# Performance work log

Measured on AMD Instinct MI355X. Metric: run time of the kernel, lower is better.

## Reference

```python
import jax, jax.numpy as jnp
import numpy as np

L = 6       # n_layers
D = 1024    # d_model
H = 16      # n_heads
HD = D // H
DF = 4096   # d_ff
E = 8       # n_experts
K = 2       # top_k
V = 32000   # vocab
B = 2
S = 1024    # seq_len == max_seq_len


def setup_inputs() -> dict:
    key = jax.random.key(0)
    ks = iter(jax.random.split(key, 40))
    n = lambda shape: jax.random.normal(next(ks), shape, dtype=jnp.float32) * 0.02
    return {
        'input_ids': jax.random.randint(next(ks), (B, S), 0, V),
        'tok_emb': n((V, D)),
        'pos_emb': n((S, D)),
        'attn_in_w': n((L, 3 * D, D)),   # packed q,k,v in_proj (torch MultiheadAttention)
        'attn_in_b': jnp.zeros((L, 3 * D), jnp.float32),
        'attn_out_w': n((L, D, D)),
        'attn_out_b': jnp.zeros((L, D), jnp.float32),
        'ln1_w': jnp.ones((L, D), jnp.float32),
        'ln1_b': jnp.zeros((L, D), jnp.float32),
        'ln2_w': jnp.ones((L, D), jnp.float32),
        'ln2_b': jnp.zeros((L, D), jnp.float32),
        'ffn_w1': n((L, DF, D)),
        'ffn_b1': jnp.zeros((L, DF), jnp.float32),
        'ffn_w2': n((L, D, DF)),
        'ffn_b2': jnp.zeros((L, D), jnp.float32),
        'gate_w': n((L // 2, E, D)),     # router gate for the 3 MoE (odd) layers
        'lnf_w': jnp.ones((D,), jnp.float32),
        'lnf_b': jnp.zeros((D,), jnp.float32),
        'head_w': n((V, D)),
    }


def _ln(x, w, b):
    m = x.mean(-1, keepdims=True)
    v = x.var(-1, keepdims=True)
    return (x - m) / jnp.sqrt(v + 1e-5) * w + b


def _mha(x, in_w, in_b, out_w, out_b):
    b_, s_, _ = x.shape
    qkv = x @ in_w.T + in_b
    q, k, v = jnp.split(qkv, 3, axis=-1)
    rs = lambda t: t.reshape(b_, s_, H, HD)
    q, k, v = rs(q), rs(k), rs(v)
    scores = jnp.einsum('bqhd,bkhd->bhqk', q, k) / np.sqrt(HD).astype(np.float32)
    causal = jnp.tril(jnp.ones((s_, s_), bool))
    scores = jnp.where(causal[None, None], scores, -jnp.inf)
    a = jax.nn.softmax(scores, axis=-1)
    o = jnp.einsum('bhqk,bkhd->bqhd', a, v).reshape(b_, s_, D)
    return o @ out_w.T + out_b


def reference(input_ids, tok_emb, pos_emb, attn_in_w, attn_in_b, attn_out_w,
              attn_out_b, ln1_w, ln1_b, ln2_w, ln2_b, ffn_w1, ffn_b1, ffn_w2,
              ffn_b2, gate_w, lnf_w, lnf_b, head_w):
    s = input_ids.shape[1]
    x = tok_emb[input_ids] + pos_emb[jnp.arange(s)][None]  # [B,S,D]
    aux = jnp.float32(0.0)
    for i in range(L):
        h = _ln(x + _mha(x, attn_in_w[i], attn_in_b[i], attn_out_w[i], attn_out_b[i]),
                ln1_w[i], ln1_b[i])
        ffn = jax.nn.relu(h @ ffn_w1[i].T + ffn_b1[i]) @ ffn_w2[i].T + ffn_b2[i]
        if i % 2 == 1:  # MoE layer; source shares ONE expert module across all experts
            gi = i // 2
            probs = jax.nn.softmax(h @ gate_w[gi].T, axis=-1)     # [B,S,E]
            topv, topi = jax.lax.top_k(probs, K)
            ffn = ffn * topv.sum(-1, keepdims=True)               # combine top-k weights
            me = probs.mean((0, 1))                               # mean gate prob per expert
            ce = jax.nn.one_hot(topi[..., 0], E, dtype=probs.dtype).mean((0, 1))
            aux = aux + E * jnp.sum(me * ce)                      # load-balancing aux loss
        x = _ln(h + ffn, ln2_w[i], ln2_b[i])
    x = _ln(x, lnf_w, lnf_b)
    logits = x @ head_w.T  # [B,S,V]
    return (logits, aux)
```

## Files before the change

### kernel.cpp

```cpp
#include <hip/hip_runtime.h>
#include <hip/hip_bf16.h>

typedef __hip_bfloat16 bf16;
typedef __bf16 bf16x8 __attribute__((ext_vector_type(8)));
typedef float f32x4 __attribute__((ext_vector_type(4)));
typedef short s16x8 __attribute__((ext_vector_type(8)));
typedef unsigned short u16;

#define NL 6
#define DM 1024
#define NH 16
#define HD 64
#define DF 4096
#define NE 8
#define NV 32000
#define NB 2
#define NS 1024
#define NT (NB*NS)

__device__ __forceinline__ float ldin(const void* p, long i, int isf32) {
    return isf32 ? ((const float*)p)[i]
                 : __bfloat162float(((const bf16*)p)[i]);
}

__global__ __launch_bounds__(256)
void cvt_k(const void* __restrict__ src, bf16* __restrict__ dst, long n,
           const u16* __restrict__ probe)
{
    int isf32 = (probe[0] != (u16)0x3F80);
    long stride = (long)gridDim.x * 256 * 8;
    for (long i = ((long)blockIdx.x * 256 + threadIdx.x) * 8; i < n; i += stride) {
        if (isf32) {
            const float* s = (const float*)src + i;
            f32x4 f0 = *(const f32x4*)s;
            f32x4 f1 = *(const f32x4*)(s + 4);
            s16x8 o;
            #pragma unroll
            for (int jj = 0; jj < 4; ++jj) {
                bf16 v0 = __float2bfloat16(f0[jj]);
                bf16 v1 = __float2bfloat16(f1[jj]);
                o[jj]   = *(short*)&v0;
                o[4+jj] = *(short*)&v1;
            }
            *(s16x8*)&dst[i] = o;
        } else {
            *(s16x8*)&dst[i] = *(const s16x8*)((const u16*)src + i);
        }
    }
}

template<int TMI, int WF32, int WB16, int RELU>
__global__ __launch_bounds__(256)
void gemm128(const u16* __restrict__ A, const u16* __restrict__ B,
             const void* __restrict__ bias, long biasoff,
             const u16* __restrict__ probe,
             float* __restrict__ Cf, bf16* __restrict__ Cb,
             int M, int N, int K, int lda, int ldb, int ldc, float alpha)
{
    int isf32 = (probe[0] != (u16)0x3F80);
    int bm = blockIdx.x, bn = blockIdx.y;

    __shared__ __align__(16) u16 As[TMI*32*64];
    __shared__ __align__(16) u16 Bs[128*64];

    int t = threadIdx.x;
    int lane = t & 63, wv = t >> 6;
    int wr = wv >> 1, wc = wv & 1;
    int rsel = lane & 15, grp = lane >> 4;

    f32x4 acc[TMI][4] = {};

    const u16* Ag = A + (long)(bm * (TMI*32)) * lda;
    const u16* Bg = B + (long)(bn * 128) * ldb;
    int sub = lane >> 3;
    int csw = ((lane & 7) ^ sub) * 8;

    for (int kt = 0; kt < K; kt += 64) {
        __syncthreads();
        #pragma unroll
        for (int i = 0; i < TMI; ++i) {
            int row = wv*(TMI*8) + i*8;
            __builtin_amdgcn_global_load_lds(
                (const __attribute__((address_space(1))) void*)(Ag + (long)(row + sub)*lda + kt + csw),
                (__attribute__((address_space(3))) void*)(As + row*64),
                16, 0, 0);
        }
        #pragma unroll
        for (int i = 0; i < 4; ++i) {
            int row = wv*32 + i*8;
            __builtin_amdgcn_global_load_lds(
                (const __attribute__((address_space(1))) void*)(Bg + (long)(row + sub)*ldb + kt + csw),
                (__attribute__((address_space(3))) void*)(Bs + row*64),
                16, 0, 0);
        }
        __syncthreads();
        #pragma unroll
        for (int kk = 0; kk < 2; ++kk) {
            int js = ((kk*4 + grp) ^ (rsel & 7)) * 8;
            bf16x8 af[TMI], bf[4];
            #pragma unroll
            for (int mi = 0; mi < TMI; ++mi)
                af[mi] = *(const bf16x8*)&As[(wr*(TMI*16) + mi*16 + rsel)*64 + js];
            #pragma unroll
            for (int ni = 0; ni < 4; ++ni)
                bf[ni] = *(const bf16x8*)&Bs[(wc*64 + ni*16 + rsel)*64 + js];
            #pragma unroll
            for (int mi = 0; mi < TMI; ++mi)
                #pragma unroll
                for (int ni = 0; ni < 4; ++ni)
                    acc[mi][ni] = __builtin_amdgcn_mfma_f32_16x16x32_bf16(
                        af[mi], bf[ni], acc[mi][ni], 0, 0, 0);
        }
    }

    #pragma unroll
    for (int mi = 0; mi < TMI; ++mi)
    #pragma unroll
    for (int ni = 0; ni < 4; ++ni)
    #pragma unroll
    for (int j = 0; j < 4; ++j) {
        int row = bm*(TMI*32) + wr*(TMI*16) + mi*16 + grp*4 + j;
        int col = bn*128 + wc*64 + ni*16 + rsel;
        float v = acc[mi][ni][j] * alpha;
        if (bias) v += ldin(bias, biasoff + col, isf32);
        if (RELU) v = fmaxf(v, 0.f);
        long ci = (long)row * ldc + col;
        if (WF32) Cf[ci] = v;
        if (WB16) Cb[ci] = __float2bfloat16(v);
    }
}

__global__ __launch_bounds__(256)
void gemm64f(const u16* __restrict__ A, const void* __restrict__ B,
             const u16* __restrict__ probe, float* __restrict__ Cf,
             int M, int N, int K, int lda, int ldb, int ldc)
{
    int isf32 = (probe[0] != (u16)0x3F80);
    int bn = blockIdx.x, bm = blockIdx.y;
    __shared__ __align__(16) u16 As[64*72];
    __shared__ __align__(16) u16 Bs[64*72];
    int t = threadIdx.x;
    int lane = t & 63, wv = t >> 6;
    int wm = (wv >> 1) * 32, wn = (wv & 1) * 32;
    int rsel = lane & 15, grp = lane >> 4;
    f32x4 acc[2][2] = {};
    const u16* Ag = A + (long)(bm * 64) * lda;
    int r0 = t >> 3, c8 = (t & 7) * 8;
    for (int kt = 0; kt < K; kt += 64) {
        __syncthreads();
        #pragma unroll
        for (int p = 0; p < 2; ++p) {
            int r = r0 + 32 * p;
            *(s16x8*)&As[r*72 + c8] = *(const s16x8*)(Ag + (long)r * lda + kt + c8);
        }
        if (isf32) {
            const float* Bg = (const float*)B + (long)(bn * 64) * ldb;
            #pragma unroll
            for (int p = 0; p < 2; ++p) {
                int r = r0 + 32 * p;
                const float* src = Bg + (long)r * ldb + kt + c8;
                f32x4 f0 = *(const f32x4*)src;
                f32x4 f1 = *(const f32x4*)(src + 4);
                s16x8 o8;
                #pragma unroll
                for (int jj = 0; jj < 4; ++jj) {
                    bf16 v0 = __float2bfloat16(f0[jj]);
                    bf16 v1 = __float2bfloat16(f1[jj]);
                    o8[jj]   = *(short*)&v0;
                    o8[4+jj] = *(short*)&v1;
                }
                *(s16x8*)&Bs[r*72 + c8] = o8;
            }
        } else {
            const u16* Bg = (const u16*)B + (long)(bn * 64) * ldb;
            #pragma unroll
            for (int p = 0; p < 2; ++p) {
                int r = r0 + 32 * p;
                *(s16x8*)&Bs[r*72 + c8] = *(const s16x8*)(Bg + (long)r * ldb + kt + c8);
            }
        }
        __syncthreads();
        #pragma unroll
        for (int kk = 0; kk < 64; kk += 32) {
            bf16x8 a0 = *(const bf16x8*)&As[(wm +      rsel)*72 + kk + grp*8];
            bf16x8 a1 = *(const bf16x8*)&As[(wm + 16 + rsel)*72 + kk + grp*8];
            bf16x8 b0 = *(const bf16x8*)&Bs[(wn +      rsel)*72 + kk + grp*8];
            bf16x8 b1 = *(const bf16x8*)&Bs[(wn + 16 + rsel)*72 + kk + grp*8];
            acc[0][0] = __builtin_amdgcn_mfma_f32_16x16x32_bf16(a0, b0, acc[0][0], 0, 0, 0);
            acc[0][1] = __builtin_amdgcn_mfma_f32_16x16x32_bf16(a0, b1, acc[0][1], 0, 0, 0);
            acc[1][0] = __builtin_amdgcn_mfma_f32_16x16x32_bf16(a1, b0, acc[1][0], 0, 0, 0);
            acc[1][1] = __builtin_amdgcn_mfma_f32_16x16x32_bf16(a1, b1, acc[1][1], 0, 0, 0);
        }
    }
    #pragma unroll
    for (int mi = 0; mi < 2; ++mi)
    #pragma unroll
    for (int ni = 0; ni < 2; ++ni)
    #pragma unroll
    for (int j = 0; j < 4; ++j) {
        int row = bm*64 + wm + 16*mi + grp*4 + j;
        int col = bn*64 + wn + 16*ni + rsel;
        Cf[(long)row * ldc + col] = acc[mi][ni][j];
    }
}

__global__ __launch_bounds__(256)
void vtrans_k(const u16* __restrict__ qkv, u16* __restrict__ vt)
{
    int st = blockIdx.x;
    int z  = blockIdx.y;
    int b = z >> 4, h = z & 15;
    __shared__ u16 T[64*72];
    int t = threadIdx.x;
    int r = t >> 3, c8 = (t & 7) * 8;
    const u16* src = qkv + (long)(b*NS + st*64) * (3*DM) + 2*DM + h*HD;
    #pragma unroll
    for (int p = 0; p < 2; ++p) {
        int s = r + p*32;
        *(s16x8*)&T[s*72 + c8] = *(const s16x8*)(src + (long)s*(3*DM) + c8);
    }
    __syncthreads();
    u16* dst = vt + (long)z*HD*NS + (long)st*64;
    #pragma unroll
    for (int p = 0; p < 2; ++p) {
        int d = r + p*32;
        u16 tmp[8];
        #pragma unroll
        for (int j = 0; j < 8; ++j) tmp[j] = T[(c8+j)*72 + d];
        *(s16x8*)(dst + (long)d*NS + c8) = *(s16x8*)tmp;
    }
}

__global__ __launch_bounds__(256)
void flash_k(const u16* __restrict__ qkv, const u16* __restrict__ vt,
             bf16* __restrict__ o)
{
    int qt = blockIdx.x;
    int z  = blockIdx.y;
    int b = z >> 4, h = z & 15;

    __shared__ __align__(16) u16 Qs[64*72];
    __shared__ __align__(16) u16 Ks[2][64*64];
    __shared__ __align__(16) u16 Vs[2][64*64];
    __shared__ __align__(16) u16 Ps[4*16*72];

    int t = threadIdx.x;
    int lane = t & 63, wv = t >> 6;
    int rsel = lane & 15, grp = lane >> 4;
    int sub = lane >> 3, csw = ((lane & 7) ^ sub) * 8;

    const u16* qbase = qkv + (long)(b*NS) * (3*DM) + h*HD;
    const u16* kbase = qbase + DM;
    const u16* vbase = vt + (long)z*HD*NS;

    {
        #pragma unroll
        for (int u = 0; u < 2; ++u) {
            int id = t + u*256;
            int r = id >> 3, c = (id & 7) * 8;
            *(s16x8*)&Qs[r*72 + c] = *(const s16x8*)(qbase + (long)(qt*64 + r)*(3*DM) + c);
        }
    }

    auto stage = [&](int buf, int kt) {
        #pragma unroll
        for (int i = 0; i < 2; ++i) {
            int row = wv*16 + i*8;
            __builtin_amdgcn_global_load_lds(
                (const __attribute__((address_space(1))) void*)(kbase + (long)(kt*64 + row + sub)*(3*DM) + csw),
                (__attribute__((address_space(3))) void*)(&Ks[buf][row*64]),
                16, 0, 0);
            __builtin_amdgcn_global_load_lds(
                (const __attribute__((address_space(1))) void*)(vbase + (long)(row + sub)*NS + kt*64 + csw),
                (__attribute__((address_space(3))) void*)(&Vs[buf][row*64]),
                16, 0, 0);
        }
    };
    stage(0, 0);
    __syncthreads();

    bf16x8 qf[2];
    #pragma unroll
    for (int kk = 0; kk < 2; ++kk)
        qf[kk] = *(const bf16x8*)&Qs[(wv*16 + rsel)*72 + kk*32 + grp*8];

    float m[4], l[4];
    f32x4 acc_o[4] = {};
    #pragma unroll
    for (int j = 0; j < 4; ++j) { m[j] = -3.0e38f; l[j] = 0.f; }

    for (int kt = 0; kt <= qt; ++kt) {
        int cur = kt & 1;

        bf16x8 kf[2][4];
        #pragma unroll
        for (int kk = 0; kk < 2; ++kk) {
            int js = ((kk*4 + grp) ^ (rsel & 7)) * 8;
            #pragma unroll
            for (int ni = 0; ni < 4; ++ni)
                kf[kk][ni] = *(const bf16x8*)&Ks[cur][(16*ni + rsel)*64 + js];
        }

        if (kt < qt) stage(cur ^ 1, kt + 1);

        f32x4 s[4] = {};
        #pragma unroll
        for (int kk = 0; kk < 2; ++kk)
            #pragma unroll
            for (int ni = 0; ni < 4; ++ni)
                s[ni] = __builtin_amdgcn_mfma_f32_16x16x32_bf16(qf[kk], kf[kk][ni], s[ni], 0, 0, 0);

        float sv[4][4];
        int rloc = wv*16 + grp*4;
        #pragma unroll
        for (int ni = 0; ni < 4; ++ni)
        #pragma unroll
        for (int j = 0; j < 4; ++j) {
            float x = s[ni][j] * 0.125f;
            if (kt == qt && (16*ni + rsel) > (rloc + j)) x = -3.0e38f;
            sv[ni][j] = x;
        }
        float pm[4];
        #pragma unroll
        for (int j = 0; j < 4; ++j)
            pm[j] = fmaxf(fmaxf(sv[0][j], sv[1][j]), fmaxf(sv[2][j], sv[3][j]));
        #pragma unroll
        for (int msk = 1; msk < 16; msk <<= 1)
            #pragma unroll
            for (int j = 0; j < 4; ++j)
                pm[j] = fmaxf(pm[j], __shfl_xor(pm[j], msk));

        float mn[4], sc[4], ps[4];
        #pragma unroll
        for (int j = 0; j < 4; ++j) {
            mn[j] = fmaxf(m[j], pm[j]);
            sc[j] = __expf(m[j] - mn[j]);
            ps[j] = 0.f;
        }
        u16* pw = &Ps[wv*16*72];
        #pragma unroll
        for (int ni = 0; ni < 4; ++ni)
        #pragma unroll
        for (int j = 0; j < 4; ++j) {
            float p = __expf(sv[ni][j] - mn[j]);
            ps[j] += p;
            bf16 pb = __float2bfloat16(p);
            pw[(grp*4 + j)*72 + 16*ni + rsel] = *(u16*)&pb;
        }
        #pragma unroll
        for (int msk = 1; msk < 16; msk <<= 1)
            #pragma unroll
            for (int j = 0; j < 4; ++j)
                ps[j] += __shfl_xor(ps[j], msk);
        #pragma unroll
        for (int j = 0; j < 4; ++j) {
            l[j] = l[j]*sc[j] + ps[j];
            m[j] = mn[j];
        }
        #pragma unroll
        for (int ni = 0; ni < 4; ++ni)
        #pragma unroll
        for (int j = 0; j < 4; ++j)
            acc_o[ni][j] *= sc[j];

        __syncthreads();

        #pragma unroll
        for (int kk = 0; kk < 2; ++kk) {
            int js = ((kk*4 + grp) ^ (rsel & 7)) * 8;
            bf16x8 pa = *(const bf16x8*)&pw[rsel*72 + kk*32 + grp*8];
            #pragma unroll
            for (int ni = 0; ni < 4; ++ni) {
                bf16x8 vf = *(const bf16x8*)&Vs[cur][(16*ni + rsel)*64 + js];
                acc_o[ni] = __builtin_amdgcn_mfma_f32_16x16x32_bf16(pa, vf, acc_o[ni], 0, 0, 0);
            }
        }
        __syncthreads();
    }

    #pragma unroll
    for (int j = 0; j < 4; ++j) {
        int q = qt*64 + wv*16 + grp*4 + j;
        float inv = 1.f / l[j];
        #pragma unroll
        for (int ni = 0; ni < 4; ++ni) {
            int d = 16*ni + rsel;
            o[(long)(b*NS + q)*DM + h*HD + d] = __float2bfloat16(acc_o[ni][j] * inv);
        }
    }
}

__global__ __launch_bounds__(256)
void embed_k(const int* __restrict__ ids, const void* __restrict__ te,
             const void* __restrict__ pe, const u16* __restrict__ probe,
             float* __restrict__ xf, bf16* __restrict__ xb)
{
    int isf32 = (probe[0] != (u16)0x3F80);
    int tk = blockIdx.x;
    int s = tk & (NS-1);
    long idb = (long)ids[tk] * DM;
    #pragma unroll
    for (int u = 0; u < 4; ++u) {
        int d = threadIdx.x + u*256;
        float v = ldin(te, idb + d, isf32) + ldin(pe, (long)s*DM + d, isf32);
        xf[(long)tk*DM + d] = v;
        xb[(long)tk*DM + d] = __float2bfloat16(v);
    }
}

__global__ __launch_bounds__(256)
void ln_k(const float* __restrict__ in1, const float* __restrict__ in2,
          const float* __restrict__ rsc, const void* __restrict__ w, long woff,
          const void* __restrict__ b, long boff, const u16* __restrict__ probe,
          float* __restrict__ of, bf16* __restrict__ ob)
{
    int isf32 = (probe[0] != (u16)0x3F80);
    int row = blockIdx.x;
    int t = threadIdx.x;
    const float* p1 = in1 + (long)row * DM;
    float sc = rsc ? rsc[row] : 1.f;
    float v[4], s = 0.f;
    #pragma unroll
    for (int u = 0; u < 4; ++u) {
        int d = t + u*256;
        float x = p1[d];
        if (in2) x += sc * in2[(long)row*DM + d];
        v[u] = x; s += x;
    }
    __shared__ float r1[4], r2[4];
    int lane = t & 63, wv = t >> 6;
    #pragma unroll
    for (int msk = 32; msk; msk >>= 1) s += __shfl_xor(s, msk);
    if (lane == 0) r1[wv] = s;
    __syncthreads();
    float mean = (r1[0]+r1[1]+r1[2]+r1[3]) * (1.f/DM);
    float vs = 0.f;
    #pragma unroll
    for (int u = 0; u < 4; ++u) { float d0 = v[u] - mean; vs += d0*d0; }
    #pragma unroll
    for (int msk = 32; msk; msk >>= 1) vs += __shfl_xor(vs, msk);
    if (lane == 0) r2[wv] = vs;
    __syncthreads();
    float var = (r2[0]+r2[1]+r2[2]+r2[3]) * (1.f/DM);
    float rstd = rsqrtf(var + 1e-5f);
    #pragma unroll
    for (int u = 0; u < 4; ++u) {
        int d = t + u*256;
        float y = (v[u] - mean) * rstd * ldin(w, woff + d, isf32) + ldin(b, boff + d, isf32);
        if (of) of[(long)row*DM + d] = y;
        if (ob) ob[(long)row*DM + d] = __float2bfloat16(y);
    }
}

__global__ __launch_bounds__(256)
void router_k(const float* __restrict__ h, const void* __restrict__ gwp, long goff,
              const u16* __restrict__ probe,
              float* __restrict__ scale, float* __restrict__ mece)
{
    int isf32 = (probe[0] != (u16)0x3F80);
    int lane = threadIdx.x & 63, wv = threadIdx.x >> 6;
    int base = blockIdx.x * 64 + wv * 16;

    float me_loc[NE], ce_loc[NE];
    #pragma unroll
    for (int e = 0; e < NE; ++e) { me_loc[e] = 0.f; ce_loc[e] = 0.f; }

    for (int j = 0; j < 16; ++j) {
        int tk = base + j;
        const float* hr = h + (long)tk * DM;
        float part[NE];
        #pragma unroll
        for (int e = 0; e < NE; ++e) part[e] = 0.f;
        #pragma unroll 4
        for (int i = 0; i < 16; ++i) {
            int d = lane + 64*i;
            float hv = hr[d];
            #pragma unroll
            for (int e = 0; e < NE; ++e)
                part[e] += hv * ldin(gwp, goff + e*DM + d, isf32);
        }
        #pragma unroll
        for (int e = 0; e < NE; ++e)
            #pragma unroll
            for (int msk = 32; msk; msk >>= 1)
                part[e] += __shfl_xor(part[e], msk);
        float mx = part[0];
        #pragma unroll
        for (int e = 1; e < NE; ++e) mx = fmaxf(mx, part[e]);
        float ex[NE], sum = 0.f;
        #pragma unroll
        for (int e = 0; e < NE; ++e) { ex[e] = __expf(part[e] - mx); sum += ex[e]; }
        float inv = 1.f / sum;
        int i1 = 0; float v1 = ex[0]*inv;
        #pragma unroll
        for (int e = 1; e < NE; ++e) { float p = ex[e]*inv; if (p > v1) { v1 = p; i1 = e; } }
        float v2 = -1.f;
        #pragma unroll
        for (int e = 0; e < NE; ++e) { float p = ex[e]*inv; if (e != i1 && p > v2) v2 = p; }
        if (lane == 0) {
            scale[tk] = v1 + v2;
            #pragma unroll
            for (int e = 0; e < NE; ++e) me_loc[e] += ex[e]*inv;
            ce_loc[i1] += 1.f;
        }
    }

    __shared__ float red[4][2*NE];
    if (lane == 0) {
        #pragma unroll
        for (int e = 0; e < NE; ++e) {
            red[wv][e]      = me_loc[e];
            red[wv][NE + e] = ce_loc[e];
        }
    }
    __syncthreads();
    if (threadIdx.x < 2*NE) {
        float s = red[0][threadIdx.x] + red[1][threadIdx.x]
                + red[2][threadIdx.x] + red[3][threadIdx.x];
        atomicAdd(&mece[threadIdx.x], s);
    }
}

__global__ void auxfin_k(const float* __restrict__ me, const float* __restrict__ ce,
                         float* __restrict__ aux)
{
    float s = 0.f;
    for (int e = 0; e < NE; ++e) s += me[e] * ce[e];
    *aux += (float)NE * s * (1.f / ((float)NT * (float)NT));
}

__global__ void zerof(float* p, int n)
{
    int i = blockIdx.x * 64 + threadIdx.x;
    if (i < n) p[i] = 0.f;
}

__global__ void write_aux_f32_k(float* dst, const float* aux)
{
    *dst = *aux;
}

extern "C" void kernel_launch(void* const* d_in, const int* in_sizes, int n_in,
                              void* d_out, int out_size, void* d_ws, size_t ws_size,
                              hipStream_t stream)
{
    const int*  ids     = (const int*)d_in[0];
    const void* tok_emb = d_in[1];
    const void* pos_emb = d_in[2];
    const void* ain_w   = d_in[3];
    const void* ain_b   = d_in[4];
    const void* aout_w  = d_in[5];
    const void* aout_b  = d_in[6];
    const u16*  probe   = (const u16*)d_in[7];
    const void* ln1w    = d_in[7];
    const void* ln1b    = d_in[8];
    const void* ln2w    = d_in[9];
    const void* ln2b    = d_in[10];
    const void* fw1     = d_in[11];
    const void* fb1     = d_in[12];
    const void* fw2     = d_in[13];
    const void* fb2     = d_in[14];
    const void* gw      = d_in[15];
    const void* lnfw    = d_in[16];
    const void* lnfb    = d_in[17];
    const void* headw   = d_in[18];
    float* out = (float*)d_out;

    char* op = (char*)d_out;
    auto oalloc = [&](size_t n) { char* p = op; op += (n + 255) & ~(size_t)255; return p; };
    bf16*  f1_b   = (bf16*) oalloc((size_t)NT*DF*2);
    bf16*  qkv_b  = (bf16*) oalloc((size_t)NT*3*DM*2);
    float* tmp_f  = (float*)oalloc((size_t)NT*DM*4);
    bf16*  o_b    = (bf16*) oalloc((size_t)NT*DM*2);
    bf16*  h_b    = (bf16*) oalloc((size_t)NT*DM*2);
    float* x_f    = (float*)oalloc((size_t)NT*DM*4);
    float* h_f    = (float*)oalloc((size_t)NT*DM*4);
    u16*   vt     = (u16*)  oalloc((size_t)NB*NH*HD*NS*2);
    bf16*  wc_ain = (bf16*) oalloc((size_t)NL*3*DM*DM*2);
    bf16*  wc_aout= (bf16*) oalloc((size_t)NL*DM*DM*2);
    bf16*  wc_fw1 = (bf16*) oalloc((size_t)NL*DF*DM*2);
    bf16*  wc_fw2 = (bf16*) oalloc((size_t)NL*DM*DF*2);

    char* wp = (char*)d_ws;
    auto alloc = [&](size_t n) { char* p = wp; wp += (n + 255) & ~(size_t)255; return p; };
    bf16*  x_b    = (bf16*) alloc((size_t)NT*DM*2);
    float* scale  = (float*)alloc((size_t)NT*4);
    float* mece   = (float*)alloc(16*4);
    float* aux    = (float*)alloc(4);
    size_t ws_used = (size_t)(wp - (char*)d_ws);
    bool head_cvt = (ws_size >= ws_used + (size_t)NV*DM*2 + 256);
    bf16* wc_head = head_cvt ? (bf16*)alloc((size_t)NV*DM*2) : nullptr;

    auto cvt = [&](const void* src, bf16* dst, long n) {
        int blocks = (int)((n/8 + 255) / 256); if (blocks > 2048) blocks = 2048;
        cvt_k<<<blocks, 256, 0, stream>>>(src, dst, n, probe);
    };

    zerof<<<1, 64, 0, stream>>>(aux, 1);
    cvt(ain_w,  wc_ain,  (long)NL*3*DM*DM);
    cvt(aout_w, wc_aout, (long)NL*DM*DM);
    cvt(fw1,    wc_fw1,  (long)NL*DF*DM);
    cvt(fw2,    wc_fw2,  (long)NL*DM*DF);
    if (head_cvt) cvt(headw, wc_head, (long)NV*DM);

    embed_k<<<NT, 256, 0, stream>>>(ids, tok_emb, pos_emb, probe, x_f, x_b);

    for (int i = 0; i < NL; ++i) {
        gemm128<4,0,1,0><<<dim3(NT/128, 3*DM/128), 256, 0, stream>>>(
            (const u16*)x_b, (const u16*)(wc_ain + (size_t)i*3*DM*DM),
            ain_b, (long)i*3*DM, probe,
            nullptr, qkv_b, NT, 3*DM, DM, DM, DM, 3*DM, 1.f);
        vtrans_k<<<dim3(NS/64, NB*NH), 256, 0, stream>>>((const u16*)qkv_b, vt);
        flash_k<<<dim3(NS/64, NB*NH), 256, 0, stream>>>((const u16*)qkv_b, vt, o_b);
        gemm128<2,1,0,0><<<dim3(NT/64, DM/128), 256, 0, stream>>>(
            (const u16*)o_b, (const u16*)(wc_aout + (size_t)i*DM*DM),
            aout_b, (long)i*DM, probe,
            tmp_f, nullptr, NT, DM, DM, DM, DM, DM, 1.f);
        ln_k<<<NT, 256, 0, stream>>>(x_f, tmp_f, nullptr, ln1w, (long)i*DM, ln1b, (long)i*DM,
                                     probe, h_f, h_b);
        gemm128<4,0,1,1><<<dim3(NT/128, DF/128), 256, 0, stream>>>(
            (const u16*)h_b, (const u16*)(wc_fw1 + (size_t)i*DF*DM),
            fb1, (long)i*DF, probe,
            nullptr, f1_b, NT, DF, DM, DM, DM, DF, 1.f);
        gemm128<2,1,0,0><<<dim3(NT/64, DM/128), 256, 0, stream>>>(
            (const u16*)f1_b, (const u16*)(wc_fw2 + (size_t)i*DM*DF),
            fb2, (long)i*DM, probe,
            tmp_f, nullptr, NT, DM, DF, DF, DF, DM, 1.f);
        const float* sc = nullptr;
        if (i & 1) {
            zerof<<<1, 64, 0, stream>>>(mece, 16);
            router_k<<<NT/64, 256, 0, stream>>>(h_f, gw, (long)(i/2)*NE*DM, probe,
                                                scale, mece);
            auxfin_k<<<1, 1, 0, stream>>>(mece, mece + 8, aux);
            sc = scale;
        }
        ln_k<<<NT, 256, 0, stream>>>(h_f, tmp_f, sc, ln2w, (long)i*DM, ln2b, (long)i*DM,
                                     probe, x_f, x_b);
    }
    ln_k<<<NT, 256, 0, stream>>>(x_f, nullptr, nullptr, lnfw, 0, lnfb, 0, probe, nullptr, x_b);
    if (head_cvt) {
        gemm128<4,1,0,0><<<dim3(NT/128, NV/128), 256, 0, stream>>>(
            (const u16*)x_b, (const u16*)wc_head, nullptr, 0, probe,
            out, nullptr, NT, NV, DM, DM, DM, NV, 1.f);
    } else {
        gemm64f<<<dim3(NV/64, NT/64), 256, 0, stream>>>(
            (const u16*)x_b, headw, probe, out, NT, NV, DM, DM, DM, NV);
    }
    write_aux_f32_k<<<1, 1, 0, stream>>>(out + (size_t)NT*NV, aux);
}
```

Baseline: 1.934 ms.

## Split causal flash attention KV range in two and merge partials

The flash attention grid gains a third dimension of 2. Each block handles half of the causal key tiles for its query tile and writes unnormalized fp32 partial outputs plus running max and sum to scratch. A new merge kernel combines the two halves with log-sum-exp rescaling and writes the bf16 output. The aim is more blocks and better balance of the triangular causal workload across CUs. The cost is extra fp32 scratch traffic and one more kernel launch per layer.

Result: slower. 1.982 ms (+2.5%).

```diff
diff --git a/kernel.cpp b/kernel.cpp
--- a/kernel.cpp
+++ b/kernel.cpp
@@ -17,6 +17,7 @@
 #define NB 2
 #define NS 1024
 #define NT (NB*NS)
+#define NBH (NB*NH)
 
 __device__ __forceinline__ float ldin(const void* p, long i, int isf32) {
     return isf32 ? ((const float*)p)[i]
@@ -233,11 +234,16 @@
 
 __global__ __launch_bounds__(256)
 void flash_k(const u16* __restrict__ qkv, const u16* __restrict__ vt,
-             bf16* __restrict__ o)
+             float* __restrict__ Of, float* __restrict__ ml)
 {
     int qt = blockIdx.x;
     int z  = blockIdx.y;
+    int sp = blockIdx.z;
     int b = z >> 4, h = z & 15;
+
+    int hh  = (qt + 2) >> 1;
+    int kt0 = sp * hh;
+    int kt1 = min(qt, kt0 + hh - 1);
 
     __shared__ __align__(16) u16 Qs[64*72];
     __shared__ __align__(16) u16 Ks[2][64*64];
@@ -253,13 +259,11 @@
     const u16* kbase = qbase + DM;
     const u16* vbase = vt + (long)z*HD*NS;
 
-    {
-        #pragma unroll
-        for (int u = 0; u < 2; ++u) {
-            int id = t + u*256;
-            int r = id >> 3, c = (id & 7) * 8;
-            *(s16x8*)&Qs[r*72 + c] = *(const s16x8*)(qbase + (long)(qt*64 + r)*(3*DM) + c);
-        }
+    #pragma unroll
+    for (int u = 0; u < 2; ++u) {
+        int id = t + u*256;
+        int r = id >> 3, c = (id & 7) * 8;
+        *(s16x8*)&Qs[r*72 + c] = *(const s16x8*)(qbase + (long)(qt*64 + r)*(3*DM) + c);
     }
 
     auto stage = [&](int buf, int kt) {
@@ -276,7 +280,7 @@
                 16, 0, 0);
         }
     };
-    stage(0, 0);
+    if (kt0 <= kt1) stage(0, kt0);
     __syncthreads();
 
     bf16x8 qf[2];
@@ -289,8 +293,8 @@
     #pragma unroll
     for (int j = 0; j < 4; ++j) { m[j] = -3.0e38f; l[j] = 0.f; }
 
-    for (int kt = 0; kt <= qt; ++kt) {
-        int cur = kt & 1;
+    for (int kt = kt0; kt <= kt1; ++kt) {
+        int cur = (kt - kt0) & 1;
 
         bf16x8 kf[2][4];
         #pragma unroll
@@ -300,8 +304,7 @@
             for (int ni = 0; ni < 4; ++ni)
                 kf[kk][ni] = *(const bf16x8*)&Ks[cur][(16*ni + rsel)*64 + js];
         }
-
-        if (kt < qt) stage(cur ^ 1, kt + 1);
+        if (kt < kt1) stage(cur ^ 1, kt + 1);
 
         f32x4 s[4] = {};
         #pragma unroll
@@ -378,16 +381,38 @@
         __syncthreads();
     }
 
+    long obase = (((long)sp*NBH + z)*NS + (long)qt*64) * HD;
+    long mbase = (((long)sp*NBH + z)*NS + (long)qt*64);
     #pragma unroll
     for (int j = 0; j < 4; ++j) {
-        int q = qt*64 + wv*16 + grp*4 + j;
-        float inv = 1.f / l[j];
-        #pragma unroll
-        for (int ni = 0; ni < 4; ++ni) {
-            int d = 16*ni + rsel;
-            o[(long)(b*NS + q)*DM + h*HD + d] = __float2bfloat16(acc_o[ni][j] * inv);
-        }
-    }
+        int r = wv*16 + grp*4 + j;
+        #pragma unroll
+        for (int ni = 0; ni < 4; ++ni)
+            Of[obase + (long)r*HD + 16*ni + rsel] = acc_o[ni][j];
+        if (rsel == 0) {
+            ml[(mbase + r)*2    ] = m[j];
+            ml[(mbase + r)*2 + 1] = l[j];
+        }
+    }
+}
+
+__global__ __launch_bounds__(256)
+void fmerge_k(const float* __restrict__ Of, const float* __restrict__ ml,
+              bf16* __restrict__ o)
+{
+    long R = (long)blockIdx.x*4 + (threadIdx.x >> 6);
+    int d = threadIdx.x & 63;
+    int z = (int)(R >> 10), q = (int)(R & (NS-1));
+    int b = z >> 4, h = z & 15;
+    long i0 = (long)z*NS + q;
+    long i1 = ((long)NBH + z)*NS + q;
+    float m0 = ml[i0*2], l0 = ml[i0*2+1];
+    float m1 = ml[i1*2], l1 = ml[i1*2+1];
+    float ms = fmaxf(m0, m1);
+    float a0 = __expf(m0 - ms), a1 = __expf(m1 - ms);
+    float O = Of[i0*HD + d]*a0 + Of[i1*HD + d]*a1;
+    float l = l0*a0 + l1*a1;
+    o[((long)(b*NS + q))*DM + h*HD + d] = __float2bfloat16(O / l);
 }
 
 __global__ __launch_bounds__(256)
@@ -575,7 +600,9 @@
     bf16*  h_b    = (bf16*) oalloc((size_t)NT*DM*2);
     float* x_f    = (float*)oalloc((size_t)NT*DM*4);
     float* h_f    = (float*)oalloc((size_t)NT*DM*4);
-    u16*   vt     = (u16*)  oalloc((size_t)NB*NH*HD*NS*2);
+    u16*   vt     = (u16*)  oalloc((size_t)NBH*HD*NS*2);
+    float* Of     = (float*)oalloc((size_t)2*NBH*NS*HD*4);
+    float* ml     = (float*)oalloc((size_t)2*NBH*NS*2*4);
     bf16*  wc_ain = (bf16*) oalloc((size_t)NL*3*DM*DM*2);
     bf16*  wc_aout= (bf16*) oalloc((size_t)NL*DM*DM*2);
     bf16*  wc_fw1 = (bf16*) oalloc((size_t)NL*DF*DM*2);
@@ -610,8 +637,9 @@
             (const u16*)x_b, (const u16*)(wc_ain + (size_t)i*3*DM*DM),
             ain_b, (long)i*3*DM, probe,
             nullptr, qkv_b, NT, 3*DM, DM, DM, DM, 3*DM, 1.f);
-        vtrans_k<<<dim3(NS/64, NB*NH), 256, 0, stream>>>((const u16*)qkv_b, vt);
-        flash_k<<<dim3(NS/64, NB*NH), 256, 0, stream>>>((const u16*)qkv_b, vt, o_b);
+        vtrans_k<<<dim3(NS/64, NBH), 256, 0, stream>>>((const u16*)qkv_b, vt);
+        flash_k<<<dim3(NS/64, NBH, 2), 256, 0, stream>>>((const u16*)qkv_b, vt, Of, ml);
+        fmerge_k<<<(NBH*NS)/4, 256, 0, stream>>>(Of, ml, o_b);
         gemm128<2,1,0,0><<<dim3(NT/64, DM/128), 256, 0, stream>>>(
             (const u16*)o_b, (const u16*)(wc_aout + (size_t)i*DM*DM),
             aout_b, (long)i*DM, probe,
```
